# Kernel optimization log

Measured on AMD Instinct MI355X. Metric: run time of the kernel, lower is better.

Reference implementation:

```python
import jax, jax.numpy as jnp
import numpy as np

B, C, T = 8, 512, 1024
H = 8
D = C // H          # head_dim = 64
K = 64              # max_rel_dist
REL = 2 * K + 1     # 129


def setup_inputs() -> dict:
    key = jax.random.key(0)
    ks = jax.random.split(key, 12)
    s = 0.02
    return {
        "x": jax.random.normal(ks[0], (B, C, T), jnp.float32),
        "x_mask": jnp.ones((B, 1, T), jnp.float32),
        "W_q": jax.random.normal(ks[1], (C, C), jnp.float32) * s,
        "b_q": jnp.zeros((C,), jnp.float32),
        "W_k": jax.random.normal(ks[2], (C, C), jnp.float32) * s,
        "b_k": jnp.zeros((C,), jnp.float32),
        "W_v": jax.random.normal(ks[3], (C, C), jnp.float32) * s,
        "b_v": jnp.zeros((C,), jnp.float32),
        "W_o": jax.random.normal(ks[4], (C, C), jnp.float32) * s,
        "b_o": jnp.zeros((C,), jnp.float32),
        "emb_rel_k": jax.random.normal(ks[5], (REL, D), jnp.float32) * 0.01,
        "emb_rel_v": jax.random.normal(ks[6], (REL, D), jnp.float32) * 0.01,
    }


def _conv1x1(x, W, b):
    # Conv1d with kernel_size=1: (B,C,T) x (Cout,Cin) -> (B,Cout,T)
    return jnp.einsum("oc,bct->bot", W, x) + b[None, :, None]


def _shape_heads(x):
    # (B,C,T) -> (B,H,T,D)
    b = x.shape[0]
    return x.reshape(b, H, D, T).transpose(0, 1, 3, 2)


def reference(x, x_mask, W_q, b_q, W_k, b_k, W_v, b_v, W_o, b_o, emb_rel_k, emb_rel_v):
    q = _shape_heads(_conv1x1(x, W_q, b_q))  # (B,H,T,D)
    k = _shape_heads(_conv1x1(x, W_k, b_k))
    v = _shape_heads(_conv1x1(x, W_v, b_v))

    # relative position indices: clamp(j - i, -K, K) + K  -> (T,T)
    pos = jnp.arange(T)
    rel_idx = jnp.clip(pos[None, :] - pos[:, None], -K, K) + K

    # scores: scaled QK^T plus unscaled relative-key term (faithful to source)
    attn = jnp.einsum("bhid,bhjd->bhij", q, k) / (D ** 0.5)
    rel_k_tt = emb_rel_k[rel_idx]            # (T,T,D)
    attn = attn + jnp.einsum("bhid,ijd->bhij", q, rel_k_tt)

    # key mask: positions with x_mask <= 0 get -1e9
    key_mask = (x_mask <= 0).reshape(x.shape[0], 1, 1, T)
    attn = jnp.where(key_mask, -1e9, attn)
    attn = jax.nn.softmax(attn, axis=-1)     # dropout p=0.0 -> identity

    y = jnp.einsum("bhij,bhjd->bhid", attn, v)
    rel_v_tt = emb_rel_v[rel_idx]            # (T,T,D)
    y = y + jnp.einsum("bhij,ijd->bhid", attn, rel_v_tt)

    # (B,H,T,D) -> (B,H,D,T) -> (B,C,T)
    y = y.transpose(0, 1, 3, 2).reshape(x.shape[0], C, T)
    y = _conv1x1(y, W_o, b_o)
    return y * x_mask
```

## Files before the change

### kernel.cpp

```cpp
#include <hip/hip_runtime.h>

#define B_   8
#define C_   512
#define T_   1024
#define H_   8
#define D_   64
#define K_   64
#define REL_ 129

typedef unsigned short u16;
typedef __attribute__((ext_vector_type(8))) short short8;
typedef __attribute__((ext_vector_type(4))) float f32x4;

__device__ __forceinline__ float b2f(u16 u) {
    return __uint_as_float(((unsigned)u) << 16);
}
__device__ __forceinline__ u16 f2b(float f) {
    unsigned x = __float_as_uint(f);
    x += 0x7fffu + ((x >> 16) & 1u);
    return (u16)(x >> 16);
}

__global__ __launch_bounds__(256) void cast_x_kernel(
    const float* __restrict__ x, u16* __restrict__ xt)
{
    __shared__ u16 tile[64][72];
    const int t0 = blockIdx.x * 64, c0 = blockIdx.y * 64, b = blockIdx.z;
    const int tid = threadIdx.x;
    const int f = tid & 15, r0 = tid >> 4;
#pragma unroll
    for (int p = 0; p < 4; ++p) {
        const int c = r0 + p * 16;
        const float4 v = *(const float4*)(x + ((size_t)b * C_ + c0 + c) * T_ + t0 + f * 4);
        tile[c][f * 4 + 0] = f2b(v.x);
        tile[c][f * 4 + 1] = f2b(v.y);
        tile[c][f * 4 + 2] = f2b(v.z);
        tile[c][f * 4 + 3] = f2b(v.w);
    }
    __syncthreads();
#pragma unroll
    for (int p = 0; p < 4; ++p) {
        const int t = r0 + p * 16;
        ushort4 u;
        u.x = tile[f * 4 + 0][t];
        u.y = tile[f * 4 + 1][t];
        u.z = tile[f * 4 + 2][t];
        u.w = tile[f * 4 + 3][t];
        *(ushort4*)(xt + ((size_t)b * T_ + t0 + t) * C_ + c0 + f * 4) = u;
    }
}

__global__ __launch_bounds__(256) void cast_w_kernel(
    const float* __restrict__ Wq, const float* __restrict__ Wk,
    const float* __restrict__ Wv, const float* __restrict__ Wo,
    u16* __restrict__ Wh)
{
    const int gid = blockIdx.x * 256 + threadIdx.x;
    const int s = gid >> 16;
    const int off = (gid & 65535) * 4;
    const float* W = (s == 0) ? Wq : (s == 1) ? Wk : (s == 2) ? Wv : Wo;
    const float4 v = *(const float4*)(W + off);
    ushort4 u;
    u.x = f2b(v.x); u.y = f2b(v.y); u.z = f2b(v.z); u.w = f2b(v.w);
    *(ushort4*)(Wh + ((size_t)s << 18) + off) = u;
}

__global__ __launch_bounds__(256) void cast_rel_kernel(
    const float* __restrict__ erk, const float* __restrict__ erv,
    u16* __restrict__ ervt, u16* __restrict__ erkb)
{
    const int idx = blockIdx.x * 256 + threadIdx.x;
    if (idx < 64 * 160) {
        const int d = idx / 160, rel = idx % 160;
        ervt[idx] = (rel < REL_) ? f2b(erv[rel * D_ + d]) : (u16)0;
    } else {
        const int j = idx - 64 * 160;
        if (j < REL_ * D_) erkb[j] = f2b(erk[j]);
    }
}

__global__ __launch_bounds__(256) void proj_mfma(
    const u16* __restrict__ xt, const u16* __restrict__ Wh,
    const float* __restrict__ bq, const float* __restrict__ bk, const float* __restrict__ bv,
    u16* __restrict__ qh, u16* __restrict__ kh, u16* __restrict__ vt)
{
    __shared__ u16 Wt[64][72];

    const int t0 = blockIdx.x * 64;
    const int h  = blockIdx.y;
    const int sel = blockIdx.z >> 3;
    const int b   = blockIdx.z & 7;
    const int tid = threadIdx.x, wave = tid >> 6, lane = tid & 63;
    const int quad = lane >> 4, l16 = lane & 15;

    const u16* Wbase = Wh + ((size_t)sel << 18) + ((size_t)(h * 64) << 9);
    const u16* A = xt + (((size_t)b * T_ + t0 + wave * 16 + l16) << 9);

    const int so = tid >> 2;
    const int sc = (tid & 3) * 16;
    const u16* wsrc = Wbase + ((size_t)so << 9) + sc;

    f32x4 acc[4] = {{0.f,0.f,0.f,0.f},{0.f,0.f,0.f,0.f},{0.f,0.f,0.f,0.f},{0.f,0.f,0.f,0.f}};

    uint4 wv0 = *(const uint4*)(wsrc);
    uint4 wv1 = *(const uint4*)(wsrc + 8);
#pragma unroll 1
    for (int i = 0; i < 8; ++i) {
        const int c0 = i * 64;
        __syncthreads();
        *(uint4*)&Wt[so][sc] = wv0;
        *(uint4*)&Wt[so][sc + 8] = wv1;
        __syncthreads();
        if (i < 7) {
            wv0 = *(const uint4*)(wsrc + c0 + 64);
            wv1 = *(const uint4*)(wsrc + c0 + 72);
        }
#pragma unroll
        for (int kk = 0; kk < 64; kk += 32) {
            const short8 af = *(const short8*)(A + c0 + kk + quad * 8);
#pragma unroll
            for (int nt = 0; nt < 4; ++nt) {
                const short8 bf = *(const short8*)(&Wt[nt * 16 + l16][kk + quad * 8]);
                acc[nt] = __builtin_amdgcn_mfma_f32_16x16x32_bf16(af, bf, acc[nt], 0, 0, 0);
            }
        }
    }

    const float* bias = (sel == 0) ? bq : (sel == 1) ? bk : bv;
    const int bh = b * 8 + h;
#pragma unroll
    for (int nt = 0; nt < 4; ++nt) {
        const int d = nt * 16 + l16;
        const float bo = bias[h * 64 + d];
#pragma unroll
        for (int rix = 0; rix < 4; ++rix) {
            const int t = t0 + wave * 16 + quad * 4 + rix;
            const u16 val = f2b(acc[nt][rix] + bo);
            if (sel == 2) {
                vt[(((size_t)bh * 64 + d) << 10) + t] = val;
            } else {
                u16* dst = sel ? kh : qh;
                dst[(((size_t)bh * T_ + t) << 6) + d] = val;
            }
        }
    }
}

__global__ __launch_bounds__(256, 2) void attn_kernel(
    const u16* __restrict__ qh, const u16* __restrict__ kh, const u16* __restrict__ vt,
    const u16* __restrict__ erkb, const u16* __restrict__ ervt,
    const float* __restrict__ xmask, u16* __restrict__ yf)
{
    __shared__ u16   Sb[32][1032];
    __shared__ u16   sw[32][168];
    __shared__ float red[4][32][2];
    __shared__ float invrow[32];

    const int gid = blockIdx.x;
    const int x8 = gid & 7, r5 = gid >> 3;
    const int bh = x8 + 8 * (r5 >> 5);
    const int i0 = (r5 & 31) * 32;
    const int b = bh >> 3, h = bh & 7;
    const int tid = threadIdx.x, wave = tid >> 6, lane = tid & 63;
    const int quad = lane >> 4, l16 = lane & 15;

    short8 qa[2][2];
#pragma unroll
    for (int g = 0; g < 2; ++g) {
        const u16* qrow = qh + (((size_t)bh * T_ + i0 + g * 16 + l16) << 6);
        qa[g][0] = *(const short8*)(qrow + quad * 8);
        qa[g][1] = *(const short8*)(qrow + 32 + quad * 8);
    }

    for (int tile = wave; tile < 9; tile += 4) {
        const int rel = tile * 16 + l16;
        const int rl = rel > 128 ? 128 : rel;
        const u16* ep = erkb + rl * 64 + quad * 8;
        const short8 b0 = *(const short8*)(ep);
        const short8 b1 = *(const short8*)(ep + 32);
#pragma unroll
        for (int g = 0; g < 2; ++g) {
            f32x4 m = {0.f, 0.f, 0.f, 0.f};
            m = __builtin_amdgcn_mfma_f32_16x16x32_bf16(qa[g][0], b0, m, 0, 0, 0);
            m = __builtin_amdgcn_mfma_f32_16x16x32_bf16(qa[g][1], b1, m, 0, 0, 0);
            if (rel < 129) {
#pragma unroll
                for (int rix = 0; rix < 4; ++rix)
                    sw[g * 16 + quad * 4 + rix][rel] = f2b(m[rix]);
            }
        }
    }
    __syncthreads();

    float psum[2][4] = {{0.f,0.f,0.f,0.f},{0.f,0.f,0.f,0.f}};
    float phi [2][4] = {{0.f,0.f,0.f,0.f},{0.f,0.f,0.f,0.f}};
    float slo_c[2][4], shi_c[2][4];
#pragma unroll
    for (int g = 0; g < 2; ++g)
#pragma unroll
        for (int rix = 0; rix < 4; ++rix) {
            const int row = g * 16 + quad * 4 + rix;
            slo_c[g][rix] = b2f(sw[row][0]);
            shi_c[g][rix] = b2f(sw[row][2 * K_]);
        }
    {
        const u16* kb = kh + ((size_t)bh << 16);
#pragma unroll
        for (int ct = 0; ct < 16; ++ct) {
            const int j0 = wave * 256 + ct * 16;
            const u16* krow = kb + ((size_t)(j0 + l16) << 6);
            const short8 kb0 = *(const short8*)(krow + quad * 8);
            const short8 kb1 = *(const short8*)(krow + 32 + quad * 8);
            const int j = j0 + l16;
            const float xmv = xmask[b * T_ + j];
#pragma unroll
            for (int g = 0; g < 2; ++g) {
                f32x4 acc = {0.f, 0.f, 0.f, 0.f};
                acc = __builtin_amdgcn_mfma_f32_16x16x32_bf16(qa[g][0], kb0, acc, 0, 0, 0);
                acc = __builtin_amdgcn_mfma_f32_16x16x32_bf16(qa[g][1], kb1, acc, 0, 0, 0);
                const int dd = j0 - (i0 + g * 16);
                if (dd <= -79) {
#pragma unroll
                    for (int rix = 0; rix < 4; ++rix) {
                        const int row = g * 16 + quad * 4 + rix;
                        float val = acc[rix] * 0.125f + slo_c[g][rix];
                        val = (xmv > 0.f) ? val : -1e9f;
                        const u16 pb = f2b(__expf(fminf(val, 30.f)));
                        const float er = b2f(pb);
                        Sb[row][j] = pb;
                        psum[g][rix] += er;
                    }
                } else if (dd >= 79) {
#pragma unroll
                    for (int rix = 0; rix < 4; ++rix) {
                        const int row = g * 16 + quad * 4 + rix;
                        float val = acc[rix] * 0.125f + shi_c[g][rix];
                        val = (xmv > 0.f) ? val : -1e9f;
                        const u16 pb = f2b(__expf(fminf(val, 30.f)));
                        const float er = b2f(pb);
                        Sb[row][j] = pb;
                        psum[g][rix] += er;
                        phi[g][rix]  += er;
                    }
                } else {
#pragma unroll
                    for (int rix = 0; rix < 4; ++rix) {
                        const int row = g * 16 + quad * 4 + rix;
                        const int i = i0 + row;
                        int rel = j - i;
                        rel = (rel < -K_) ? -K_ : (rel > K_) ? K_ : rel;
                        float val = acc[rix] * 0.125f + b2f(sw[row][rel + K_]);
                        val = (xmv > 0.f) ? val : -1e9f;
                        const u16 pb = f2b(__expf(fminf(val, 30.f)));
                        const float er = b2f(pb);
                        Sb[row][j] = pb;
                        psum[g][rix] += er;
                        phi[g][rix]  += (j >= i + K_) ? er : 0.f;
                    }
                }
            }
        }
#pragma unroll
        for (int m = 1; m < 16; m <<= 1)
#pragma unroll
            for (int g = 0; g < 2; ++g)
#pragma unroll
                for (int rix = 0; rix < 4; ++rix) {
                    psum[g][rix] += __shfl_xor(psum[g][rix], m);
                    phi[g][rix]  += __shfl_xor(phi[g][rix], m);
                }
        if (l16 == 0)
#pragma unroll
            for (int g = 0; g < 2; ++g)
#pragma unroll
                for (int rix = 0; rix < 4; ++rix) {
                    const int row = g * 16 + quad * 4 + rix;
                    red[wave][row][0] = psum[g][rix];
                    red[wave][row][1] = phi[g][rix];
                }
    }
    __syncthreads();

    {
        const int rr = tid >> 3;
        const int c0 = tid & 7;
        const float sumrow = red[0][rr][0] + red[1][rr][0] + red[2][rr][0] + red[3][rr][0];
        const float phirow = red[0][rr][1] + red[1][rr][1] + red[2][rr][1] + red[3][rr][1];
        float intsum = 0.f;
        for (int rel = c0; rel < 168; rel += 8) {
            if (rel == 0 || rel == 2 * K_) continue;
            u16 v = 0;
            if (rel < 2 * K_) {
                const int j = i0 + rr + rel - K_;
                if (j >= 0 && j < T_) v = Sb[rr][j];
                intsum += b2f(v);
            }
            sw[rr][rel] = v;
        }
        intsum += __shfl_xor(intsum, 1);
        intsum += __shfl_xor(intsum, 2);
        intsum += __shfl_xor(intsum, 4);
        if (c0 == 0) {
            sw[rr][2 * K_] = f2b(phirow);
            sw[rr][0]      = f2b(sumrow - intsum - phirow);
            invrow[rr]     = 1.0f / sumrow;
        }
    }
    __syncthreads();

    {
        const int dh = wave * 16 + l16;
        const u16* vb = vt + ((size_t)bh << 16) + ((size_t)dh << 10);
        f32x4 og0 = {0.f, 0.f, 0.f, 0.f}, og1 = {0.f, 0.f, 0.f, 0.f};
#pragma unroll 4
        for (int ks = 0; ks < 32; ++ks) {
            const short8 af = *(const short8*)(vb + (ks << 5) + quad * 8);
            const short8 p0 = *(const short8*)(&Sb[l16][ks * 32 + quad * 8]);
            const short8 p1 = *(const short8*)(&Sb[16 + l16][ks * 32 + quad * 8]);
            og0 = __builtin_amdgcn_mfma_f32_16x16x32_bf16(af, p0, og0, 0, 0, 0);
            og1 = __builtin_amdgcn_mfma_f32_16x16x32_bf16(af, p1, og1, 0, 0, 0);
        }
        const u16* ep = ervt + dh * 160;
#pragma unroll
        for (int kt = 0; kt < 5; ++kt) {
            const short8 af = *(const short8*)(ep + kt * 32 + quad * 8);
            const short8 p0 = *(const short8*)(&sw[l16][kt * 32 + quad * 8]);
            const short8 p1 = *(const short8*)(&sw[16 + l16][kt * 32 + quad * 8]);
            og0 = __builtin_amdgcn_mfma_f32_16x16x32_bf16(af, p0, og0, 0, 0, 0);
            og1 = __builtin_amdgcn_mfma_f32_16x16x32_bf16(af, p1, og1, 0, 0, 0);
        }
        const float iv0 = invrow[l16];
        const float iv1 = invrow[16 + l16];
        const int dbase = (h << 6) + wave * 16 + quad * 4;
        ushort4 u0, u1;
        u0.x = f2b(og0[0] * iv0); u0.y = f2b(og0[1] * iv0);
        u0.z = f2b(og0[2] * iv0); u0.w = f2b(og0[3] * iv0);
        u1.x = f2b(og1[0] * iv1); u1.y = f2b(og1[1] * iv1);
        u1.z = f2b(og1[2] * iv1); u1.w = f2b(og1[3] * iv1);
        *(ushort4*)(yf + (((size_t)b * T_ + i0 + l16) << 9) + dbase) = u0;
        *(ushort4*)(yf + (((size_t)b * T_ + i0 + 16 + l16) << 9) + dbase) = u1;
    }
}

__global__ __launch_bounds__(256) void outproj_mfma(
    const u16* __restrict__ yf, const u16* __restrict__ Woh, const float* __restrict__ bo,
    const float* __restrict__ xmask, float* __restrict__ out)
{
    __shared__ u16 Yt[64][72];

    const int o0 = blockIdx.x * 64;
    const int b  = blockIdx.y >> 4;
    const int t0 = (blockIdx.y & 15) * 64;
    const int tid = threadIdx.x, wave = tid >> 6, lane = tid & 63;
    const int quad = lane >> 4, l16 = lane & 15;

    const u16* A = Woh + ((size_t)(o0 + wave * 16 + l16) << 9);

    const int so = tid >> 2;
    const int sc = (tid & 3) * 16;
    const u16* ysrc = yf + (((size_t)b * T_ + t0 + so) << 9) + sc;

    f32x4 acc[4] = {{0.f,0.f,0.f,0.f},{0.f,0.f,0.f,0.f},{0.f,0.f,0.f,0.f},{0.f,0.f,0.f,0.f}};

    uint4 wv0 = *(const uint4*)(ysrc);
    uint4 wv1 = *(const uint4*)(ysrc + 8);
#pragma unroll 1
    for (int i = 0; i < 8; ++i) {
        const int c0 = i * 64;
        __syncthreads();
        *(uint4*)&Yt[so][sc] = wv0;
        *(uint4*)&Yt[so][sc + 8] = wv1;
        __syncthreads();
        if (i < 7) {
            wv0 = *(const uint4*)(ysrc + c0 + 64);
            wv1 = *(const uint4*)(ysrc + c0 + 72);
        }
#pragma unroll
        for (int kk = 0; kk < 64; kk += 32) {
            const short8 af = *(const short8*)(A + c0 + kk + quad * 8);
#pragma unroll
            for (int nt = 0; nt < 4; ++nt) {
                const short8 bf = *(const short8*)(&Yt[nt * 16 + l16][kk + quad * 8]);
                acc[nt] = __builtin_amdgcn_mfma_f32_16x16x32_bf16(af, bf, acc[nt], 0, 0, 0);
            }
        }
    }

#pragma unroll
    for (int nt = 0; nt < 4; ++nt) {
        const int t = t0 + nt * 16 + l16;
        const float xmv = xmask[b * T_ + t];
#pragma unroll
        for (int rix = 0; rix < 4; ++rix) {
            const int o = o0 + wave * 16 + quad * 4 + rix;
            out[((size_t)b * C_ + o) * T_ + t] = (acc[nt][rix] + bo[o]) * xmv;
        }
    }
}

extern "C" void kernel_launch(void* const* d_in, const int* in_sizes, int n_in,
                              void* d_out, int out_size, void* d_ws, size_t ws_size,
                              hipStream_t stream) {
    const float* x     = (const float*)d_in[0];
    const float* xmask = (const float*)d_in[1];
    const float* Wq    = (const float*)d_in[2];
    const float* bq    = (const float*)d_in[3];
    const float* Wk    = (const float*)d_in[4];
    const float* bk    = (const float*)d_in[5];
    const float* Wv    = (const float*)d_in[6];
    const float* bv    = (const float*)d_in[7];
    const float* Wo    = (const float*)d_in[8];
    const float* bo    = (const float*)d_in[9];
    const float* erk   = (const float*)d_in[10];
    const float* erv   = (const float*)d_in[11];

    const size_t need = 44077184;
    if (ws_size < need) return;
    u16* xt   = (u16*)d_ws;
    u16* Wh   = (u16*)((char*)d_ws + 8388608);
    u16* qh   = (u16*)((char*)d_ws + 10485760);
    u16* kh   = (u16*)((char*)d_ws + 18874368);
    u16* vt   = (u16*)((char*)d_ws + 27262976);
    u16* yf   = (u16*)((char*)d_ws + 35651584);
    u16* ervt = (u16*)((char*)d_ws + 44040192);
    u16* erkb = (u16*)((char*)d_ws + 44060672);
    float* out = (float*)d_out;

    cast_x_kernel<<<dim3(T_ / 64, C_ / 64, B_), 256, 0, stream>>>(x, xt);
    cast_w_kernel<<<dim3(1024), 256, 0, stream>>>(Wq, Wk, Wv, Wo, Wh);
    cast_rel_kernel<<<dim3(73), 256, 0, stream>>>(erk, erv, ervt, erkb);
    proj_mfma<<<dim3(T_ / 64, H_, 3 * B_), 256, 0, stream>>>(
        xt, Wh, bq, bk, bv, qh, kh, vt);
    attn_kernel<<<dim3(2048), 256, 0, stream>>>(
        qh, kh, vt, erkb, ervt, xmask, yf);
    outproj_mfma<<<dim3(C_ / 64, B_ * (T_ / 64)), 256, 0, stream>>>(
        yf, Wh + ((size_t)3 << 18), bo, xmask, out);
}
```

Measured before the change: 249.5 us.

## Fuse PV accumulation into score loop with cross-wave reduction; merge cast kernels

```diff
diff --git a/kernel.cpp b/kernel.cpp
--- a/kernel.cpp
+++ b/kernel.cpp
@@ -21,61 +21,58 @@
     return (u16)(x >> 16);
 }
 
-__global__ __launch_bounds__(256) void cast_x_kernel(
-    const float* __restrict__ x, u16* __restrict__ xt)
+__global__ __launch_bounds__(256) void cast_all_kernel(
+    const float* __restrict__ x,
+    const float* __restrict__ Wq, const float* __restrict__ Wk,
+    const float* __restrict__ Wv, const float* __restrict__ Wo,
+    const float* __restrict__ erk, const float* __restrict__ erv,
+    u16* __restrict__ xt, u16* __restrict__ Wh,
+    u16* __restrict__ ervt, u16* __restrict__ erkb)
 {
     __shared__ u16 tile[64][72];
-    const int t0 = blockIdx.x * 64, c0 = blockIdx.y * 64, b = blockIdx.z;
+    const int blk = blockIdx.x;
     const int tid = threadIdx.x;
-    const int f = tid & 15, r0 = tid >> 4;
-#pragma unroll
-    for (int p = 0; p < 4; ++p) {
-        const int c = r0 + p * 16;
-        const float4 v = *(const float4*)(x + ((size_t)b * C_ + c0 + c) * T_ + t0 + f * 4);
-        tile[c][f * 4 + 0] = f2b(v.x);
-        tile[c][f * 4 + 1] = f2b(v.y);
-        tile[c][f * 4 + 2] = f2b(v.z);
-        tile[c][f * 4 + 3] = f2b(v.w);
-    }
-    __syncthreads();
-#pragma unroll
-    for (int p = 0; p < 4; ++p) {
-        const int t = r0 + p * 16;
+    if (blk < 1024) {
+        const int t0 = (blk & 15) * 64, c0 = ((blk >> 4) & 7) * 64, b = blk >> 7;
+        const int f = tid & 15, r0 = tid >> 4;
+#pragma unroll
+        for (int p = 0; p < 4; ++p) {
+            const int c = r0 + p * 16;
+            const float4 v = *(const float4*)(x + ((size_t)b * C_ + c0 + c) * T_ + t0 + f * 4);
+            tile[c][f * 4 + 0] = f2b(v.x);
+            tile[c][f * 4 + 1] = f2b(v.y);
+            tile[c][f * 4 + 2] = f2b(v.z);
+            tile[c][f * 4 + 3] = f2b(v.w);
+        }
+        __syncthreads();
+#pragma unroll
+        for (int p = 0; p < 4; ++p) {
+            const int t = r0 + p * 16;
+            ushort4 u;
+            u.x = tile[f * 4 + 0][t];
+            u.y = tile[f * 4 + 1][t];
+            u.z = tile[f * 4 + 2][t];
+            u.w = tile[f * 4 + 3][t];
+            *(ushort4*)(xt + ((size_t)b * T_ + t0 + t) * C_ + c0 + f * 4) = u;
+        }
+    } else if (blk < 2048) {
+        const int gid = (blk - 1024) * 256 + tid;
+        const int s = gid >> 16;
+        const int off = (gid & 65535) * 4;
+        const float* W = (s == 0) ? Wq : (s == 1) ? Wk : (s == 2) ? Wv : Wo;
+        const float4 v = *(const float4*)(W + off);
         ushort4 u;
-        u.x = tile[f * 4 + 0][t];
-        u.y = tile[f * 4 + 1][t];
-        u.z = tile[f * 4 + 2][t];
-        u.w = tile[f * 4 + 3][t];
-        *(ushort4*)(xt + ((size_t)b * T_ + t0 + t) * C_ + c0 + f * 4) = u;
-    }
-}
-
-__global__ __launch_bounds__(256) void cast_w_kernel(
-    const float* __restrict__ Wq, const float* __restrict__ Wk,
-    const float* __restrict__ Wv, const float* __restrict__ Wo,
-    u16* __restrict__ Wh)
-{
-    const int gid = blockIdx.x * 256 + threadIdx.x;
-    const int s = gid >> 16;
-    const int off = (gid & 65535) * 4;
-    const float* W = (s == 0) ? Wq : (s == 1) ? Wk : (s == 2) ? Wv : Wo;
-    const float4 v = *(const float4*)(W + off);
-    ushort4 u;
-    u.x = f2b(v.x); u.y = f2b(v.y); u.z = f2b(v.z); u.w = f2b(v.w);
-    *(ushort4*)(Wh + ((size_t)s << 18) + off) = u;
-}
-
-__global__ __launch_bounds__(256) void cast_rel_kernel(
-    const float* __restrict__ erk, const float* __restrict__ erv,
-    u16* __restrict__ ervt, u16* __restrict__ erkb)
-{
-    const int idx = blockIdx.x * 256 + threadIdx.x;
-    if (idx < 64 * 160) {
-        const int d = idx / 160, rel = idx % 160;
-        ervt[idx] = (rel < REL_) ? f2b(erv[rel * D_ + d]) : (u16)0;
+        u.x = f2b(v.x); u.y = f2b(v.y); u.z = f2b(v.z); u.w = f2b(v.w);
+        *(ushort4*)(Wh + ((size_t)s << 18) + off) = u;
     } else {
-        const int j = idx - 64 * 160;
-        if (j < REL_ * D_) erkb[j] = f2b(erk[j]);
+        const int idx = (blk - 2048) * 256 + tid;
+        if (idx < 64 * 160) {
+            const int d = idx / 160, rel = idx % 160;
+            ervt[idx] = (rel < REL_) ? f2b(erv[rel * D_ + d]) : (u16)0;
+        } else {
+            const int j = idx - 64 * 160;
+            if (j < REL_ * D_) erkb[j] = f2b(erk[j]);
+        }
     }
 }
 
@@ -192,8 +189,6 @@
     }
     __syncthreads();
 
-    float psum[2][4] = {{0.f,0.f,0.f,0.f},{0.f,0.f,0.f,0.f}};
-    float phi [2][4] = {{0.f,0.f,0.f,0.f},{0.f,0.f,0.f,0.f}};
     float slo_c[2][4], shi_c[2][4];
 #pragma unroll
     for (int g = 0; g < 2; ++g)
@@ -203,61 +198,84 @@
             slo_c[g][rix] = b2f(sw[row][0]);
             shi_c[g][rix] = b2f(sw[row][2 * K_]);
         }
+
+    float psum[2][4] = {{0.f,0.f,0.f,0.f},{0.f,0.f,0.f,0.f}};
+    float phi [2][4] = {{0.f,0.f,0.f,0.f},{0.f,0.f,0.f,0.f}};
+    f32x4 og[4][2];
+#pragma unroll
+    for (int s = 0; s < 4; ++s)
+#pragma unroll
+        for (int g = 0; g < 2; ++g) og[s][g] = (f32x4){0.f, 0.f, 0.f, 0.f};
+
     {
         const u16* kb = kh + ((size_t)bh << 16);
-#pragma unroll
-        for (int ct = 0; ct < 16; ++ct) {
-            const int j0 = wave * 256 + ct * 16;
-            const u16* krow = kb + ((size_t)(j0 + l16) << 6);
-            const short8 kb0 = *(const short8*)(krow + quad * 8);
-            const short8 kb1 = *(const short8*)(krow + 32 + quad * 8);
-            const int j = j0 + l16;
-            const float xmv = xmask[b * T_ + j];
-#pragma unroll
-            for (int g = 0; g < 2; ++g) {
-                f32x4 acc = {0.f, 0.f, 0.f, 0.f};
-                acc = __builtin_amdgcn_mfma_f32_16x16x32_bf16(qa[g][0], kb0, acc, 0, 0, 0);
-                acc = __builtin_amdgcn_mfma_f32_16x16x32_bf16(qa[g][1], kb1, acc, 0, 0, 0);
-                const int dd = j0 - (i0 + g * 16);
-                if (dd <= -79) {
-#pragma unroll
-                    for (int rix = 0; rix < 4; ++rix) {
-                        const int row = g * 16 + quad * 4 + rix;
-                        float val = acc[rix] * 0.125f + slo_c[g][rix];
-                        val = (xmv > 0.f) ? val : -1e9f;
-                        const u16 pb = f2b(__expf(fminf(val, 30.f)));
-                        const float er = b2f(pb);
-                        Sb[row][j] = pb;
-                        psum[g][rix] += er;
-                    }
-                } else if (dd >= 79) {
-#pragma unroll
-                    for (int rix = 0; rix < 4; ++rix) {
-                        const int row = g * 16 + quad * 4 + rix;
-                        float val = acc[rix] * 0.125f + shi_c[g][rix];
-                        val = (xmv > 0.f) ? val : -1e9f;
-                        const u16 pb = f2b(__expf(fminf(val, 30.f)));
-                        const float er = b2f(pb);
-                        Sb[row][j] = pb;
-                        psum[g][rix] += er;
-                        phi[g][rix]  += er;
-                    }
-                } else {
-#pragma unroll
-                    for (int rix = 0; rix < 4; ++rix) {
-                        const int row = g * 16 + quad * 4 + rix;
-                        const int i = i0 + row;
-                        int rel = j - i;
-                        rel = (rel < -K_) ? -K_ : (rel > K_) ? K_ : rel;
-                        float val = acc[rix] * 0.125f + b2f(sw[row][rel + K_]);
-                        val = (xmv > 0.f) ? val : -1e9f;
-                        const u16 pb = f2b(__expf(fminf(val, 30.f)));
-                        const float er = b2f(pb);
-                        Sb[row][j] = pb;
-                        psum[g][rix] += er;
-                        phi[g][rix]  += (j >= i + K_) ? er : 0.f;
+        const u16* vbase = vt + ((size_t)bh << 16);
+#pragma unroll 1
+        for (int c = 0; c < 8; ++c) {
+#pragma unroll
+            for (int half = 0; half < 2; ++half) {
+                const int ct = c * 2 + half;
+                const int j0 = wave * 256 + ct * 16;
+                const u16* krow = kb + ((size_t)(j0 + l16) << 6);
+                const short8 kb0 = *(const short8*)(krow + quad * 8);
+                const short8 kb1 = *(const short8*)(krow + 32 + quad * 8);
+                const int j = j0 + l16;
+                const float xmv = xmask[b * T_ + j];
+#pragma unroll
+                for (int g = 0; g < 2; ++g) {
+                    f32x4 acc = {0.f, 0.f, 0.f, 0.f};
+                    acc = __builtin_amdgcn_mfma_f32_16x16x32_bf16(qa[g][0], kb0, acc, 0, 0, 0);
+                    acc = __builtin_amdgcn_mfma_f32_16x16x32_bf16(qa[g][1], kb1, acc, 0, 0, 0);
+                    const int dd = j0 - (i0 + g * 16);
+                    if (dd <= -79) {
+#pragma unroll
+                        for (int rix = 0; rix < 4; ++rix) {
+                            const int row = g * 16 + quad * 4 + rix;
+                            float val = acc[rix] * 0.125f + slo_c[g][rix];
+                            val = (xmv > 0.f) ? val : -1e9f;
+                            const u16 pb = f2b(__expf(fminf(val, 30.f)));
+                            const float er = b2f(pb);
+                            Sb[row][j] = pb;
+                            psum[g][rix] += er;
+                        }
+                    } else if (dd >= 79) {
+#pragma unroll
+                        for (int rix = 0; rix < 4; ++rix) {
+                            const int row = g * 16 + quad * 4 + rix;
+                            float val = acc[rix] * 0.125f + shi_c[g][rix];
+                            val = (xmv > 0.f) ? val : -1e9f;
+                            const u16 pb = f2b(__expf(fminf(val, 30.f)));
+                            const float er = b2f(pb);
+                            Sb[row][j] = pb;
+                            psum[g][rix] += er;
+                            phi[g][rix]  += er;
+                        }
+                    } else {
+#pragma unroll
+                        for (int rix = 0; rix < 4; ++rix) {
+                            const int row = g * 16 + quad * 4 + rix;
+                            const int i = i0 + row;
+                            int rel = j - i;
+                            rel = (rel < -K_) ? -K_ : (rel > K_) ? K_ : rel;
+                            float val = acc[rix] * 0.125f + b2f(sw[row][rel + K_]);
+                            val = (xmv > 0.f) ? val : -1e9f;
+                            const u16 pb = f2b(__expf(fminf(val, 30.f)));
+                            const float er = b2f(pb);
+                            Sb[row][j] = pb;
+                            psum[g][rix] += er;
+                            phi[g][rix]  += (j >= i + K_) ? er : 0.f;
+                        }
                     }
                 }
+            }
+            const int kc = wave * 256 + c * 32;
+            const short8 pb0 = *(const short8*)(&Sb[l16][kc + quad * 8]);
+            const short8 pb1 = *(const short8*)(&Sb[16 + l16][kc + quad * 8]);
+#pragma unroll
+            for (int s = 0; s < 4; ++s) {
+                const short8 af = *(const short8*)(vbase + ((size_t)(s * 16 + l16) << 10) + kc + quad * 8);
+                og[s][0] = __builtin_amdgcn_mfma_f32_16x16x32_bf16(af, pb0, og[s][0], 0, 0, 0);
+                og[s][1] = __builtin_amdgcn_mfma_f32_16x16x32_bf16(af, pb1, og[s][1], 0, 0, 0);
             }
         }
 #pragma unroll
@@ -308,37 +326,46 @@
     }
     __syncthreads();
 
+    float* fog = (float*)&Sb[0][0];
+#pragma unroll
+    for (int s = 0; s < 4; ++s)
+#pragma unroll
+        for (int g = 0; g < 2; ++g)
+            *(f32x4*)&fog[wave * 2048 + ((s * 2 + g) * 64 + lane) * 4] = og[s][g];
+    __syncthreads();
+
     {
         const int dh = wave * 16 + l16;
-        const u16* vb = vt + ((size_t)bh << 16) + ((size_t)dh << 10);
-        f32x4 og0 = {0.f, 0.f, 0.f, 0.f}, og1 = {0.f, 0.f, 0.f, 0.f};
-#pragma unroll 4
-        for (int ks = 0; ks < 32; ++ks) {
-            const short8 af = *(const short8*)(vb + (ks << 5) + quad * 8);
-            const short8 p0 = *(const short8*)(&Sb[l16][ks * 32 + quad * 8]);
-            const short8 p1 = *(const short8*)(&Sb[16 + l16][ks * 32 + quad * 8]);
-            og0 = __builtin_amdgcn_mfma_f32_16x16x32_bf16(af, p0, og0, 0, 0, 0);
-            og1 = __builtin_amdgcn_mfma_f32_16x16x32_bf16(af, p1, og1, 0, 0, 0);
-        }
         const u16* ep = ervt + dh * 160;
+        f32x4 accg[2];
+#pragma unroll
+        for (int g = 0; g < 2; ++g) {
+            const int base = ((wave * 2 + g) * 64 + lane) * 4;
+            f32x4 a0 = *(const f32x4*)&fog[base];
+            f32x4 a1 = *(const f32x4*)&fog[2048 + base];
+            f32x4 a2 = *(const f32x4*)&fog[4096 + base];
+            f32x4 a3 = *(const f32x4*)&fog[6144 + base];
+#pragma unroll
+            for (int rix = 0; rix < 4; ++rix)
+                accg[g][rix] = (a0[rix] + a1[rix]) + (a2[rix] + a3[rix]);
+        }
 #pragma unroll
         for (int kt = 0; kt < 5; ++kt) {
             const short8 af = *(const short8*)(ep + kt * 32 + quad * 8);
             const short8 p0 = *(const short8*)(&sw[l16][kt * 32 + quad * 8]);
             const short8 p1 = *(const short8*)(&sw[16 + l16][kt * 32 + quad * 8]);
-            og0 = __builtin_amdgcn_mfma_f32_16x16x32_bf16(af, p0, og0, 0, 0, 0);
-            og1 = __builtin_amdgcn_mfma_f32_16x16x32_bf16(af, p1, og1, 0, 0, 0);
-        }
-        const float iv0 = invrow[l16];
-        const float iv1 = invrow[16 + l16];
+            accg[0] = __builtin_amdgcn_mfma_f32_16x16x32_bf16(af, p0, accg[0], 0, 0, 0);
+            accg[1] = __builtin_amdgcn_mfma_f32_16x16x32_bf16(af, p1, accg[1], 0, 0, 0);
+        }
         const int dbase = (h << 6) + wave * 16 + quad * 4;
-        ushort4 u0, u1;
-        u0.x = f2b(og0[0] * iv0); u0.y = f2b(og0[1] * iv0);
-        u0.z = f2b(og0[2] * iv0); u0.w = f2b(og0[3] * iv0);
-        u1.x = f2b(og1[0] * iv1); u1.y = f2b(og1[1] * iv1);
-        u1.z = f2b(og1[2] * iv1); u1.w = f2b(og1[3] * iv1);
-        *(ushort4*)(yf + (((size_t)b * T_ + i0 + l16) << 9) + dbase) = u0;
-        *(ushort4*)(yf + (((size_t)b * T_ + i0 + 16 + l16) << 9) + dbase) = u1;
+#pragma unroll
+        for (int g = 0; g < 2; ++g) {
+            const float iv = invrow[g * 16 + l16];
+            ushort4 u;
+            u.x = f2b(accg[g][0] * iv); u.y = f2b(accg[g][1] * iv);
+            u.z = f2b(accg[g][2] * iv); u.w = f2b(accg[g][3] * iv);
+            *(ushort4*)(yf + (((size_t)b * T_ + i0 + g * 16 + l16) << 9) + dbase) = u;
+        }
     }
 }
 
@@ -426,9 +453,8 @@
     u16* erkb = (u16*)((char*)d_ws + 44060672);
     float* out = (float*)d_out;
 
-    cast_x_kernel<<<dim3(T_ / 64, C_ / 64, B_), 256, 0, stream>>>(x, xt);
-    cast_w_kernel<<<dim3(1024), 256, 0, stream>>>(Wq, Wk, Wv, Wo, Wh);
-    cast_rel_kernel<<<dim3(73), 256, 0, stream>>>(erk, erv, ervt, erkb);
+    cast_all_kernel<<<dim3(2121), 256, 0, stream>>>(
+        x, Wq, Wk, Wv, Wo, erk, erv, xt, Wh, ervt, erkb);
     proj_mfma<<<dim3(T_ / 64, H_, 3 * B_), 256, 0, stream>>>(
         xt, Wh, bq, bk, bv, qh, kh, vt);
     attn_kernel<<<dim3(2048), 256, 0, stream>>>(
```

Measured after the change: 237.5 us. 4.8% less time.
